# Kernel tuning notes

Measured on AMD Instinct MI355X. Metric: run time of the kernel, lower is better.

The kernel has to match this reference:

```python
import jax, jax.numpy as jnp
import numpy as np


def setup_inputs() -> dict:
    key = jax.random.key(0)
    ks = jax.random.split(key, 6)
    B, L, F, C, H, D1 = 262144, 20, 7, 16, 16, 8
    s = 0.1
    return {
        "x": jax.random.normal(ks[0], (B, L, F), dtype=jnp.float32),
        "conv_w": jax.random.normal(ks[1], (3, F, C), dtype=jnp.float32) * s,
        "conv_b": jnp.zeros((C,), dtype=jnp.float32),
        "rnn_w": jax.random.normal(ks[2], (C, H), dtype=jnp.float32) * s,
        "rnn_u": jax.random.normal(ks[3], (H, H), dtype=jnp.float32) * s,
        "rnn_b": jnp.zeros((H,), dtype=jnp.float32),
        "d1_w": jax.random.normal(ks[4], (H, D1), dtype=jnp.float32) * s,
        "d1_b": jnp.zeros((D1,), dtype=jnp.float32),
        "out_w": jax.random.normal(ks[5], (D1, 1), dtype=jnp.float32) * s,
        "out_b": jnp.zeros((1,), dtype=jnp.float32),
    }


def reference(x, conv_w, conv_b, rnn_w, rnn_u, rnn_b, d1_w, d1_b, out_w, out_b):
    # Conv1D, kernel 3, 'same' padding, relu.  x: [B,L,F] -> [B,L,C]
    h = jax.lax.conv_general_dilated(
        x, conv_w, window_strides=(1,), padding="SAME",
        dimension_numbers=("NWC", "WIO", "NWC"))
    h = jax.nn.relu(h + conv_b)

    # SimpleRNN(16), tanh, return last state.  Precompute input projections.
    xw = jnp.einsum("blc,ch->blh", h, rnn_w) + rnn_b  # [B,L,H]
    xw_t = jnp.swapaxes(xw, 0, 1)                      # [L,B,H]

    def step(state, xt):
        new = jnp.tanh(xt + state @ rnn_u)
        return new, None

    h0 = jnp.zeros((x.shape[0], rnn_u.shape[0]), dtype=x.dtype)
    h_last, _ = jax.lax.scan(step, h0, xw_t)           # [B,H]

    z = jax.nn.relu(h_last @ d1_w + d1_b)              # [B,8]
    return z @ out_w + out_b                           # [B,1]
```

## Files before the change

### kernel.cpp

```cpp
#include <hip/hip_runtime.h>


#define BLK 256
#define LSEQ 20
#define EPB 128
#define EPD 92
#define LOG2E2 2.8853900817779268f

typedef _Float16 f16;
typedef __fp16   fp16x2 __attribute__((ext_vector_type(2)));
typedef _Float16 f16x4 __attribute__((ext_vector_type(4)));
typedef _Float16 f16x8 __attribute__((ext_vector_type(8)));
typedef float    f32x4 __attribute__((ext_vector_type(4)));

union UB128 { uint4 q; f16x8 v; };
union UB64  { f16x4 v; fp16x2 p[2]; };
union HU    { fp16x2 p; uint u; };

__global__ __launch_bounds__(BLK, 3) void hybrid_fwd(
    const float* __restrict__ x,
    const float* __restrict__ conv_w, const float* __restrict__ conv_b,
    const float* __restrict__ rnn_w,  const float* __restrict__ rnn_u,
    const float* __restrict__ rnn_b,
    const float* __restrict__ d1_w,   const float* __restrict__ d1_b,
    const float* __restrict__ out_w,  const float* __restrict__ out_b,
    float* __restrict__ out)
{
    __shared__ __align__(16) uint xs[EPB * EPD];

    const int tid  = threadIdx.x;
    const int wave = tid >> 6, lane = tid & 63;
    const int b16  = lane & 15, g = lane >> 4;
    const long BE  = (long)blockIdx.x * EPB;

    const int e = tid >> 1;
    const int q = tid & 1;

    {
        uint* eb = xs + e * EPD;
        const uint C = 0x3C000000u;
        if (q == 0) {
            uint4 z; z.x = 0u; z.y = 0u; z.z = 0u; z.w = C;
            *(uint4*)(eb + 0) = z;
            *(uint2*)(eb + 84) = make_uint2(0u, 0u);
        } else {
            *(uint2*)(eb + 86) = make_uint2(0u, C);
            uint4 z; z.x = 0u; z.y = 0u; z.z = 0u; z.w = C;
            *(uint4*)(eb + 88) = z;
        }
    }
    {
        const float2* sp = (const float2*)(x + BE * 140 + e * 140 + q * 70);
        float2 f2[35];
        #pragma unroll
        for (int i = 0; i < 35; ++i) f2[i] = sp[i];
        const float* f = (const float*)f2;
        uint* eb = xs + e * EPD;
        #pragma unroll
        for (int i = 0; i < 10; ++i) {
            HU h0, h1, h2, h3;
            h0.p = __builtin_amdgcn_cvt_pkrtz(f[7 * i + 0], f[7 * i + 1]);
            h1.p = __builtin_amdgcn_cvt_pkrtz(f[7 * i + 2], f[7 * i + 3]);
            h2.p = __builtin_amdgcn_cvt_pkrtz(f[7 * i + 4], f[7 * i + 5]);
            h3.p = __builtin_amdgcn_cvt_pkrtz(f[7 * i + 6], 1.0f);
            uint4 val; val.x = h0.u; val.y = h1.u; val.z = h2.u; val.w = h3.u;
            *(uint4*)(eb + 4 * (10 * q + i + 1)) = val;
        }
    }
    __syncthreads();

    f16x8 A1;
    #pragma unroll
    for (int t = 0; t < 8; ++t) {
        float wv = conv_w[min(g * 7 + t, 20) * 16 + b16];
        float sel = (g < 3 && t < 7) ? wv
                  : ((g == 3 && t == 7) ? conv_b[b16] : 0.f);
        A1[t] = (f16)sel;
    }
    f16x4 A2, AU;
    f32x4 rbp;
    #pragma unroll
    for (int t = 0; t < 4; ++t) {
        A2[t]  = (f16)(LOG2E2 * rnn_w[(4 * g + t) * 16 + b16]);
        AU[t]  = (f16)(LOG2E2 * rnn_u[(4 * g + t) * 16 + b16]);
        rbp[t] = LOG2E2 * rnn_b[4 * g + t];
    }
    const f32x4 zero4 = {0.f, 0.f, 0.f, 0.f};

    const uint* rb0 = xs + (wave * 32 + b16) * EPD + 4 * g;
    const uint* rb1 = rb0 + 16 * EPD;

    f16x4 B2sA[LSEQ], B2sB[LSEQ];
    #pragma unroll
    for (int l = 0; l < LSEQ; ++l) {
        UB128 B1a, B1b;
        B1a.q = *(const uint4*)(rb0 + 4 * l);
        B1b.q = *(const uint4*)(rb1 + 4 * l);
        f32x4 a1a = __builtin_amdgcn_mfma_f32_16x16x32_f16(A1, B1a.v, zero4, 0, 0, 0);
        f32x4 a1b = __builtin_amdgcn_mfma_f32_16x16x32_f16(A1, B1b.v, zero4, 0, 0, 0);
        UB64 Ba, Bb;
        Ba.p[0] = __builtin_amdgcn_cvt_pkrtz(fmaxf(a1a[0], 0.f), fmaxf(a1a[1], 0.f));
        Ba.p[1] = __builtin_amdgcn_cvt_pkrtz(fmaxf(a1a[2], 0.f), fmaxf(a1a[3], 0.f));
        Bb.p[0] = __builtin_amdgcn_cvt_pkrtz(fmaxf(a1b[0], 0.f), fmaxf(a1b[1], 0.f));
        Bb.p[1] = __builtin_amdgcn_cvt_pkrtz(fmaxf(a1b[2], 0.f), fmaxf(a1b[3], 0.f));
        B2sA[l] = Ba.v;
        B2sB[l] = Bb.v;
    }

    f16x4 H0 = {}, H1 = {};
    #pragma unroll
    for (int l = 0; l < LSEQ; ++l) {
        f32x4 a20 = __builtin_amdgcn_mfma_f32_16x16x16f16(A2, B2sA[l], rbp, 0, 0, 0);
        f32x4 a21 = __builtin_amdgcn_mfma_f32_16x16x16f16(A2, B2sB[l], rbp, 0, 0, 0);
        a20 = __builtin_amdgcn_mfma_f32_16x16x16f16(AU, H0, a20, 0, 0, 0);
        a21 = __builtin_amdgcn_mfma_f32_16x16x16f16(AU, H1, a21, 0, 0, 0);
        float t00 = __builtin_amdgcn_rcpf(1.f + __builtin_amdgcn_exp2f(a20[0]));
        float t01 = __builtin_amdgcn_rcpf(1.f + __builtin_amdgcn_exp2f(a20[1]));
        float t02 = __builtin_amdgcn_rcpf(1.f + __builtin_amdgcn_exp2f(a20[2]));
        float t03 = __builtin_amdgcn_rcpf(1.f + __builtin_amdgcn_exp2f(a20[3]));
        float t10 = __builtin_amdgcn_rcpf(1.f + __builtin_amdgcn_exp2f(a21[0]));
        float t11 = __builtin_amdgcn_rcpf(1.f + __builtin_amdgcn_exp2f(a21[1]));
        float t12 = __builtin_amdgcn_rcpf(1.f + __builtin_amdgcn_exp2f(a21[2]));
        float t13 = __builtin_amdgcn_rcpf(1.f + __builtin_amdgcn_exp2f(a21[3]));
        UB64 Hn0, Hn1;
        Hn0.p[0] = __builtin_amdgcn_cvt_pkrtz(fmaf(-2.f, t00, 1.f), fmaf(-2.f, t01, 1.f));
        Hn0.p[1] = __builtin_amdgcn_cvt_pkrtz(fmaf(-2.f, t02, 1.f), fmaf(-2.f, t03, 1.f));
        Hn1.p[0] = __builtin_amdgcn_cvt_pkrtz(fmaf(-2.f, t10, 1.f), fmaf(-2.f, t11, 1.f));
        Hn1.p[1] = __builtin_amdgcn_cvt_pkrtz(fmaf(-2.f, t12, 1.f), fmaf(-2.f, t13, 1.f));
        H0 = Hn0.v;
        H1 = Hn1.v;
    }

    f16x4 A3;
    f32x4 c3;
    #pragma unroll
    for (int t = 0; t < 4; ++t) {
        int j = 4 * g + t;
        A3[t] = (f16)(b16 < 8 ? d1_w[j * 8 + b16] : 0.f);
        c3[t] = d1_b[min(j, 7)];
    }
    f32x4 a30 = __builtin_amdgcn_mfma_f32_16x16x16f16(A3, H0, c3, 0, 0, 0);
    f32x4 a31 = __builtin_amdgcn_mfma_f32_16x16x16f16(A3, H1, c3, 0, 0, 0);
    float p0 = 0.f, p1 = 0.f;
    #pragma unroll
    for (int r = 0; r < 4; ++r) {
        int d = 4 * g + r;
        float wv = (g < 2) ? out_w[min(d, 7)] : 0.f;
        p0 = fmaf(fmaxf(a30[r], 0.f), wv, p0);
        p1 = fmaf(fmaxf(a31[r], 0.f), wv, p1);
    }
    p0 += __shfl_xor(p0, 16); p0 += __shfl_xor(p0, 32);
    p1 += __shfl_xor(p1, 16); p1 += __shfl_xor(p1, 32);
    if (lane < 16) {
        float ob = out_b[0];
        out[BE + wave * 32 + b16]      = p0 + ob;
        out[BE + wave * 32 + 16 + b16] = p1 + ob;
    }
}

extern "C" void kernel_launch(void* const* d_in, const int* in_sizes, int n_in,
                              void* d_out, int out_size, void* d_ws, size_t ws_size,
                              hipStream_t stream) {
    const float* x      = (const float*)d_in[0];
    const float* conv_w = (const float*)d_in[1];
    const float* conv_b = (const float*)d_in[2];
    const float* rnn_w  = (const float*)d_in[3];
    const float* rnn_u  = (const float*)d_in[4];
    const float* rnn_b  = (const float*)d_in[5];
    const float* d1_w   = (const float*)d_in[6];
    const float* d1_b   = (const float*)d_in[7];
    const float* out_w  = (const float*)d_in[8];
    const float* out_b  = (const float*)d_in[9];
    float* out = (float*)d_out;

    const int B = out_size;
    const int grid = B / EPB;
    hybrid_fwd<<<grid, BLK, 0, stream>>>(x, conv_w, conv_b, rnn_w, rnn_u, rnn_b,
                                         d1_w, d1_b, out_w, out_b, out);
}
```

Baseline: 43.60 us.

## Halve block size, compact shared-memory padding, hoist epilogue weight loads

Blocks now hold 64 elements (128 threads) instead of 128, with launch bounds asking for 4 blocks per CU instead of 3. Each element's shared-memory row shrinks from 92 to 84 words: only one leading pad row per element plus a single shared trailing pad, since the zero pad after one element doubles as the leading pad of the next. The dense-layer and output weight loads are hoisted above the barrier so their global-load latency overlaps the staging of x. The intent is higher occupancy and less LDS per block, with smaller blocks and possible bank-conflict changes from the new 84-word stride as the trade-off.

```diff
diff --git a/kernel.cpp b/kernel.cpp
--- a/kernel.cpp
+++ b/kernel.cpp
@@ -1,10 +1,10 @@
 #include <hip/hip_runtime.h>
 
 
-#define BLK 256
+#define BLK 128
 #define LSEQ 20
-#define EPB 128
-#define EPD 92
+#define EPB 64
+#define EPW 84
 #define LOG2E2 2.8853900817779268f
 
 typedef _Float16 f16;
@@ -17,7 +17,7 @@
 union UB64  { f16x4 v; fp16x2 p[2]; };
 union HU    { fp16x2 p; uint u; };
 
-__global__ __launch_bounds__(BLK, 3) void hybrid_fwd(
+__global__ __launch_bounds__(BLK, 4) void hybrid_fwd(
     const float* __restrict__ x,
     const float* __restrict__ conv_w, const float* __restrict__ conv_b,
     const float* __restrict__ rnn_w,  const float* __restrict__ rnn_u,
@@ -26,7 +26,7 @@
     const float* __restrict__ out_w,  const float* __restrict__ out_b,
     float* __restrict__ out)
 {
-    __shared__ __align__(16) uint xs[EPB * EPD];
+    __shared__ __align__(16) uint xs[EPB * EPW + 8];
 
     const int tid  = threadIdx.x;
     const int wave = tid >> 6, lane = tid & 63;
@@ -36,18 +36,11 @@
     const int e = tid >> 1;
     const int q = tid & 1;
 
+    const uint4 PAD = make_uint4(0u, 0u, 0u, 0x3C000000u);
     {
-        uint* eb = xs + e * EPD;
-        const uint C = 0x3C000000u;
-        if (q == 0) {
-            uint4 z; z.x = 0u; z.y = 0u; z.z = 0u; z.w = C;
-            *(uint4*)(eb + 0) = z;
-            *(uint2*)(eb + 84) = make_uint2(0u, 0u);
-        } else {
-            *(uint2*)(eb + 86) = make_uint2(0u, C);
-            uint4 z; z.x = 0u; z.y = 0u; z.z = 0u; z.w = C;
-            *(uint4*)(eb + 88) = z;
-        }
+        uint* eb = xs + e * EPW;
+        if (q == 0) *(uint4*)eb = PAD;
+        if (tid < 2) *(uint4*)(xs + EPB * EPW + 4 * tid) = PAD;
     }
     {
         const float2* sp = (const float2*)(x + BE * 140 + e * 140 + q * 70);
@@ -55,7 +48,7 @@
         #pragma unroll
         for (int i = 0; i < 35; ++i) f2[i] = sp[i];
         const float* f = (const float*)f2;
-        uint* eb = xs + e * EPD;
+        uint* eb = xs + e * EPW;
         #pragma unroll
         for (int i = 0; i < 10; ++i) {
             HU h0, h1, h2, h3;
@@ -67,7 +60,6 @@
             *(uint4*)(eb + 4 * (10 * q + i + 1)) = val;
         }
     }
-    __syncthreads();
 
     f16x8 A1;
     #pragma unroll
@@ -85,10 +77,25 @@
         AU[t]  = (f16)(LOG2E2 * rnn_u[(4 * g + t) * 16 + b16]);
         rbp[t] = LOG2E2 * rnn_b[4 * g + t];
     }
+    f16x4 A3;
+    f32x4 c3;
+    #pragma unroll
+    for (int t = 0; t < 4; ++t) {
+        int j = 4 * g + t;
+        A3[t] = (f16)(b16 < 8 ? d1_w[j * 8 + b16] : 0.f);
+        c3[t] = d1_b[min(j, 7)];
+    }
+    float ow[4];
+    #pragma unroll
+    for (int r = 0; r < 4; ++r)
+        ow[r] = (g < 2) ? out_w[min(4 * g + r, 7)] : 0.f;
+    const float ob = out_b[0];
     const f32x4 zero4 = {0.f, 0.f, 0.f, 0.f};
 
-    const uint* rb0 = xs + (wave * 32 + b16) * EPD + 4 * g;
-    const uint* rb1 = rb0 + 16 * EPD;
+    __syncthreads();
+
+    const uint* rb0 = xs + (wave * 32 + b16) * EPW + 4 * g;
+    const uint* rb1 = rb0 + 16 * EPW;
 
     f16x4 B2sA[LSEQ], B2sB[LSEQ];
     #pragma unroll
@@ -131,28 +138,17 @@
         H1 = Hn1.v;
     }
 
-    f16x4 A3;
-    f32x4 c3;
-    #pragma unroll
-    for (int t = 0; t < 4; ++t) {
-        int j = 4 * g + t;
-        A3[t] = (f16)(b16 < 8 ? d1_w[j * 8 + b16] : 0.f);
-        c3[t] = d1_b[min(j, 7)];
-    }
     f32x4 a30 = __builtin_amdgcn_mfma_f32_16x16x16f16(A3, H0, c3, 0, 0, 0);
     f32x4 a31 = __builtin_amdgcn_mfma_f32_16x16x16f16(A3, H1, c3, 0, 0, 0);
     float p0 = 0.f, p1 = 0.f;
     #pragma unroll
     for (int r = 0; r < 4; ++r) {
-        int d = 4 * g + r;
-        float wv = (g < 2) ? out_w[min(d, 7)] : 0.f;
-        p0 = fmaf(fmaxf(a30[r], 0.f), wv, p0);
-        p1 = fmaf(fmaxf(a31[r], 0.f), wv, p1);
+        p0 = fmaf(fmaxf(a30[r], 0.f), ow[r], p0);
+        p1 = fmaf(fmaxf(a31[r], 0.f), ow[r], p1);
     }
     p0 += __shfl_xor(p0, 16); p0 += __shfl_xor(p0, 32);
     p1 += __shfl_xor(p1, 16); p1 += __shfl_xor(p1, 32);
     if (lane < 16) {
-        float ob = out_b[0];
         out[BE + wave * 32 + b16]      = p0 + ob;
         out[BE + wave * 32 + 16 + b16] = p1 + ob;
     }
```

New measurement: 47.77 us. 1.1x slower.
